# Performance work log

Measured on AMD Instinct MI355X. Metric: run time of the kernel, lower is better.

## Reference

```python
import jax, jax.numpy as jnp
import numpy as np
from math import comb

N_VARS = 6
DEGREE = 4
NUM_TERMS = 768
D1 = DEGREE + 1          # coeffs per variable row (input)
D2 = 2 * DEGREE + 1      # coeffs per variable row after squaring


def _bern_mul_weights(d):
    # Bernstein-basis product: c_k = sum_i C(d,i)C(d,k-i)/C(2d,k) a_i b_{k-i}
    W = np.zeros((d + 1, d + 1, 2 * d + 1), dtype=np.float32)
    for i in range(d + 1):
        for j in range(d + 1):
            W[i, j, i + j] = comb(d, i) * comb(d, j) / comb(2 * d, i + j)
    return W

_W_NP = _bern_mul_weights(DEGREE)          # (D1, D1, D2) product weights
_E_NP = _W_NP.sum(axis=1)                  # (D1, D2) degree elevation d -> 2d (multiply by ones poly)


def ibf_minmax(P):
    """Interval bounds of an implicit-Bernstein-form poly P: (T, V, D1).
    Per term: interval of each var row (Bernstein coeff min/max bound the poly on [0,1]),
    interval product across vars, then interval sum across terms."""
    lo = P.min(-1)  # (T, V)
    hi = P.max(-1)
    T = P.shape[0]
    ones = jnp.ones((T,), P.dtype)

    def step(carry, x):
        clo, chi = carry
        xlo, xhi = x
        cand = jnp.stack([clo * xlo, clo * xhi, chi * xlo, chi * xhi])
        return (cand.min(0), cand.max(0)), None

    (tlo, thi), _ = jax.lax.scan(step, (ones, ones), (lo.T, hi.T))  # scan over V vars
    return tlo.sum(), thi.sum()


def relu_coeffs_under(l, u):
    # quadratic lower relaxation of ReLU on [l,u]: q(x) = (x^2 - l x)/(u - l)
    den = jnp.where(u - l > 0, u - l, jnp.ones_like(u))
    quad = jnp.stack([1.0 / den, -l / den, jnp.zeros_like(l)])
    lin = jnp.array([0.0, 1.0, 0.0], dtype=quad.dtype)
    zero = jnp.zeros(3, dtype=quad.dtype)
    return jnp.where(l >= 0, lin, jnp.where(u <= 0, zero, quad))


def relu_coeffs_over(l, u):
    # quadratic upper relaxation: q(x) = u (x - l)^2 / (u - l)^2
    den = jnp.where(u - l > 0, u - l, jnp.ones_like(u))
    d2 = den * den
    quad = jnp.stack([u / d2, -2.0 * u * l / d2, u * l * l / d2])
    lin = jnp.array([0.0, 1.0, 0.0], dtype=quad.dtype)
    zero = jnp.zeros(3, dtype=quad.dtype)
    return jnp.where(l >= 0, lin, jnp.where(u <= 0, zero, quad))


def quad_of_poly(P, coeffs):
    """Compose quadratic a x^2 + b x + c with IBF poly P (T, V, D1).
    Returns IBF poly with T^2 + T + 1 terms, per-var degree 2*DEGREE."""
    a, b, c = coeffs[0], coeffs[1], coeffs[2]
    W = jnp.asarray(_W_NP)
    E = jnp.asarray(_E_NP)
    T, V, _ = P.shape
    # P^2: all pairwise term products; per-var Bernstein row product
    sq = jnp.einsum('tvi,svj,ijk->tsvk', P, P, W).reshape(T * T, V, D2)
    sq = sq.at[:, 0, :].multiply(a)          # scale by a on first var row
    # b * P: elevate each row from degree d to 2d, scale by b
    lin = jnp.einsum('tvi,ik->tvk', P, E)
    lin = lin.at[:, 0, :].multiply(b)
    # constant term c: all-ones rows, first row scaled by c
    const = jnp.ones((1, V, D2), P.dtype).at[0, 0, :].multiply(c)
    out = jnp.concatenate([sq, lin, const], axis=0)  # (T^2+T+1, V, D2)
    return out.reshape((T * T + T + 1) * V, D2)


def setup_inputs() -> dict:
    key = jax.random.key(0)
    k1, k2 = jax.random.split(key)
    input_under = jax.random.normal(k1, (NUM_TERMS * N_VARS, D1), dtype=jnp.float32)
    input_over = jax.random.normal(k2, (NUM_TERMS * N_VARS, D1), dtype=jnp.float32)
    return {"input_under": input_under, "input_over": input_over}


def reference(input_under, input_over):
    Pu = input_under.reshape(input_under.shape[0] // N_VARS, N_VARS, D1)
    Po = input_over.reshape(input_over.shape[0] // N_VARS, N_VARS, D1)
    l = ibf_minmax(Pu)[0]
    u = ibf_minmax(Po)[1]
    # torch.tensor([l, u]) detaches in the original -> stop_gradient for faithfulness
    l = jax.lax.stop_gradient(l)
    u = jax.lax.stop_gradient(u)
    cu = relu_coeffs_under(l, u)
    co = relu_coeffs_over(l, u)
    relu_node_under = quad_of_poly(Pu, cu)
    relu_node_over = quad_of_poly(Po, co)
    return relu_node_under, relu_node_over
```

## Files before the change

### kernel.cpp

```cpp
#include <hip/hip_runtime.h>

#define T_TERMS 768
#define NV 6
#define D1 5
#define D2 9
#define T2 (T_TERMS * T_TERMS)
#define PTOT (T2 + T_TERMS + 1)
#define NROWS ((unsigned int)PTOT * NV)
#define NOUT (NROWS * (unsigned int)D2)

typedef float f4 __attribute__((ext_vector_type(4)));

__global__ void bounds_kernel(const float* __restrict__ Pu,
                              const float* __restrict__ Po,
                              float* __restrict__ coef) {
    int t = threadIdx.x;
    float tlo = 0.f, thi = 0.f;
    if (t < T_TERMS) {
        float clo_u = 1.f, chi_u = 1.f;
        float clo_o = 1.f, chi_o = 1.f;
        const float* pu = Pu + t * NV * D1;
        const float* po = Po + t * NV * D1;
        #pragma unroll
        for (int v = 0; v < NV; ++v) {
            float lo = pu[v * 5 + 0], hi = lo;
            #pragma unroll
            for (int i = 1; i < 5; ++i) {
                float x = pu[v * 5 + i];
                lo = fminf(lo, x); hi = fmaxf(hi, x);
            }
            float a = clo_u * lo, b = clo_u * hi, c = chi_u * lo, d = chi_u * hi;
            clo_u = fminf(fminf(a, b), fminf(c, d));
            chi_u = fmaxf(fmaxf(a, b), fmaxf(c, d));
            lo = po[v * 5 + 0]; hi = lo;
            #pragma unroll
            for (int i = 1; i < 5; ++i) {
                float x = po[v * 5 + i];
                lo = fminf(lo, x); hi = fmaxf(hi, x);
            }
            a = clo_o * lo; b = clo_o * hi; c = chi_o * lo; d = chi_o * hi;
            clo_o = fminf(fminf(a, b), fminf(c, d));
            chi_o = fmaxf(fmaxf(a, b), fmaxf(c, d));
        }
        tlo = clo_u;
        thi = chi_o;
    }
    __shared__ float slo[12], shi[12];
    for (int off = 32; off; off >>= 1) {
        tlo += __shfl_down(tlo, off);
        thi += __shfl_down(thi, off);
    }
    int wave = threadIdx.x >> 6;
    if ((threadIdx.x & 63) == 0) { slo[wave] = tlo; shi[wave] = thi; }
    __syncthreads();
    if (threadIdx.x == 0) {
        float l = 0.f, u = 0.f;
        #pragma unroll
        for (int w = 0; w < 12; ++w) { l += slo[w]; u += shi[w]; }
        float den = (u - l > 0.f) ? (u - l) : 1.f;
        float au, bu, cu, ao, bo, co;
        if (l >= 0.f) {
            au = 0.f; bu = 1.f; cu = 0.f;
            ao = 0.f; bo = 1.f; co = 0.f;
        } else if (u <= 0.f) {
            au = bu = cu = 0.f;
            ao = bo = co = 0.f;
        } else {
            au = 1.f / den; bu = -l / den; cu = 0.f;
            float d2 = den * den;
            ao = u / d2; bo = -2.f * u * l / d2; co = u * l * l / d2;
        }
        coef[0] = au; coef[1] = bu; coef[2] = cu;
        coef[3] = ao; coef[4] = bo; coef[5] = co;
    }
}

__global__ __launch_bounds__(256) void expand_kernel(
        const float* __restrict__ Pu,
        const float* __restrict__ Po,
        const float* __restrict__ coef,
        float* __restrict__ out) {
    __shared__ float lds[256 * D2];
    static constexpr float Wt[5][5] = {
        {1.0f,        4.0f/8.0f,   6.0f/28.0f,  4.0f/56.0f,  1.0f/70.0f},
        {4.0f/8.0f,   16.0f/28.0f, 24.0f/56.0f, 16.0f/70.0f, 4.0f/56.0f},
        {6.0f/28.0f,  24.0f/56.0f, 36.0f/70.0f, 24.0f/56.0f, 6.0f/28.0f},
        {4.0f/56.0f,  16.0f/70.0f, 24.0f/56.0f, 16.0f/28.0f, 4.0f/8.0f},
        {1.0f/70.0f,  4.0f/56.0f,  6.0f/28.0f,  4.0f/8.0f,   1.0f}
    };

    const unsigned tid = threadIdx.x;
    const unsigned bid = blockIdx.x;
    const unsigned ten = blockIdx.y;
    const float* __restrict__ P = ten ? Po : Pu;
    const float* __restrict__ c3 = coef + ten * 3;

    const unsigned rr = bid * 256u + tid;
    const unsigned nvalid = min(256u, NROWS - bid * 256u);

    float c[9] = {0.f,0.f,0.f,0.f,0.f,0.f,0.f,0.f,0.f};
    if (rr < NROWS) {
        unsigned p = rr / 6u;
        unsigned v = rr - p * 6u;
        float a[5], b[5];
        float scale = 1.f;
        if (p < (unsigned)T2) {
            unsigned t = p / (unsigned)T_TERMS;
            unsigned s = p - t * (unsigned)T_TERMS;
            const float* A = P + (t * NV + v) * D1;
            const float* B = P + (s * NV + v) * D1;
            #pragma unroll
            for (int i = 0; i < 5; ++i) { a[i] = A[i]; b[i] = B[i]; }
            if (v == 0u) scale = c3[0];
        } else if (p < (unsigned)(T2 + T_TERMS)) {
            unsigned t = p - (unsigned)T2;
            const float* A = P + (t * NV + v) * D1;
            #pragma unroll
            for (int i = 0; i < 5; ++i) { a[i] = A[i]; b[i] = 1.f; }
            if (v == 0u) scale = c3[1];
        } else {
            #pragma unroll
            for (int i = 0; i < 5; ++i) { a[i] = 1.f; b[i] = 1.f; }
            if (v == 0u) scale = c3[2];
        }
        #pragma unroll
        for (int i = 0; i < 5; ++i) a[i] *= scale;
        #pragma unroll
        for (int i = 0; i < 5; ++i)
            #pragma unroll
            for (int j = 0; j < 5; ++j)
                c[i + j] = fmaf(Wt[i][j] * a[i], b[j], c[i + j]);
    }
    #pragma unroll
    for (int k = 0; k < 9; ++k) lds[tid * 9u + k] = c[k];
    __syncthreads();

    float* __restrict__ o = out + (size_t)ten * NOUT + (size_t)bid * (256u * D2);
    const unsigned nd = nvalid * 9u;
    if (nvalid == 256u) {
        const f4* l4 = (const f4*)lds;
        f4* o4 = (f4*)o;
        __builtin_nontemporal_store(l4[tid], o4 + tid);
        __builtin_nontemporal_store(l4[tid + 256u], o4 + tid + 256u);
        if (tid < 64u)
            __builtin_nontemporal_store(l4[tid + 512u], o4 + tid + 512u);
    } else {
        for (unsigned x = tid; x < nd; x += 256u)
            __builtin_nontemporal_store(lds[x], o + x);
    }
}

extern "C" void kernel_launch(void* const* d_in, const int* in_sizes, int n_in,
                              void* d_out, int out_size, void* d_ws, size_t ws_size,
                              hipStream_t stream) {
    const float* Pu = (const float*)d_in[0];
    const float* Po = (const float*)d_in[1];
    float* coef = (float*)d_ws;
    float* out = (float*)d_out;

    bounds_kernel<<<1, 768, 0, stream>>>(Pu, Po, coef);

    unsigned int blocks_x = (NROWS + 255u) / 256u;
    dim3 grid(blocks_x, 2, 1);
    expand_kernel<<<grid, 256, 0, stream>>>(Pu, Po, coef, out);
}
```

Before: 268.9 us.

## Restructure expand kernel into 768-thread tiles with LDS-staged operands and aligned stores

The expand kernel now uses 768-thread blocks that each cover one outer term t and 128 inner terms. The inner-term block and the t row are staged cooperatively in LDS, replacing per-thread divisions and scattered global loads. The linear and constant tail rows are handled by separate tail blocks. Output stores drop the nontemporal hint, and the second tensor, whose base is only 8-byte aligned, is written with realigned float4 stores. The bounds kernel also loads each term's rows as float2 vectors. This adds more LDS traffic, an extra barrier, and more complex store indexing.

Measured after the change: 256.5 us. -4.6%, faster.

```diff
diff --git a/kernel.cpp b/kernel.cpp
--- a/kernel.cpp
+++ b/kernel.cpp
@@ -8,42 +8,57 @@
 #define PTOT (T2 + T_TERMS + 1)
 #define NROWS ((unsigned int)PTOT * NV)
 #define NOUT (NROWS * (unsigned int)D2)
+#define SQ_BLOCKS 4608u
+#define TAIL_ROW0 ((unsigned int)T2 * NV)
+#define TAIL_BLOCKS 7u
+#define GRID_X (SQ_BLOCKS + TAIL_BLOCKS)
+#define BLK_DWORDS (768u * D2)
 
 typedef float f4 __attribute__((ext_vector_type(4)));
-
-__global__ void bounds_kernel(const float* __restrict__ Pu,
-                              const float* __restrict__ Po,
-                              float* __restrict__ coef) {
+typedef float f2 __attribute__((ext_vector_type(2)));
+
+__global__ void bounds_coef_kernel(const float* __restrict__ Pu,
+                                   const float* __restrict__ Po,
+                                   float* __restrict__ ws) {
     int t = threadIdx.x;
     float tlo = 0.f, thi = 0.f;
     if (t < T_TERMS) {
-        float clo_u = 1.f, chi_u = 1.f;
-        float clo_o = 1.f, chi_o = 1.f;
-        const float* pu = Pu + t * NV * D1;
-        const float* po = Po + t * NV * D1;
+        f2 r[15];
+        const f2* p2 = (const f2*)(Pu + t * (NV * D1));
+        #pragma unroll
+        for (int i = 0; i < 15; ++i) r[i] = p2[i];
+        const float* rf = (const float*)r;
+        float clo = 1.f, chi = 1.f;
         #pragma unroll
         for (int v = 0; v < NV; ++v) {
-            float lo = pu[v * 5 + 0], hi = lo;
+            float lo = rf[v * 5 + 0], hi = lo;
             #pragma unroll
             for (int i = 1; i < 5; ++i) {
-                float x = pu[v * 5 + i];
+                float x = rf[v * 5 + i];
                 lo = fminf(lo, x); hi = fmaxf(hi, x);
             }
-            float a = clo_u * lo, b = clo_u * hi, c = chi_u * lo, d = chi_u * hi;
-            clo_u = fminf(fminf(a, b), fminf(c, d));
-            chi_u = fmaxf(fmaxf(a, b), fmaxf(c, d));
-            lo = po[v * 5 + 0]; hi = lo;
+            float a = clo * lo, b = clo * hi, c = chi * lo, d = chi * hi;
+            clo = fminf(fminf(a, b), fminf(c, d));
+            chi = fmaxf(fmaxf(a, b), fmaxf(c, d));
+        }
+        tlo = clo;
+        const f2* q2 = (const f2*)(Po + t * (NV * D1));
+        #pragma unroll
+        for (int i = 0; i < 15; ++i) r[i] = q2[i];
+        clo = 1.f; chi = 1.f;
+        #pragma unroll
+        for (int v = 0; v < NV; ++v) {
+            float lo = rf[v * 5 + 0], hi = lo;
             #pragma unroll
             for (int i = 1; i < 5; ++i) {
-                float x = po[v * 5 + i];
+                float x = rf[v * 5 + i];
                 lo = fminf(lo, x); hi = fmaxf(hi, x);
             }
-            a = clo_o * lo; b = clo_o * hi; c = chi_o * lo; d = chi_o * hi;
-            clo_o = fminf(fminf(a, b), fminf(c, d));
-            chi_o = fmaxf(fmaxf(a, b), fmaxf(c, d));
-        }
-        tlo = clo_u;
-        thi = chi_o;
+            float a = clo * lo, b = clo * hi, c = chi * lo, d = chi * hi;
+            clo = fminf(fminf(a, b), fminf(c, d));
+            chi = fmaxf(fmaxf(a, b), fmaxf(c, d));
+        }
+        thi = chi;
     }
     __shared__ float slo[12], shi[12];
     for (int off = 32; off; off >>= 1) {
@@ -70,17 +85,17 @@
             float d2 = den * den;
             ao = u / d2; bo = -2.f * u * l / d2; co = u * l * l / d2;
         }
-        coef[0] = au; coef[1] = bu; coef[2] = cu;
-        coef[3] = ao; coef[4] = bo; coef[5] = co;
+        ws[0] = au; ws[1] = bu; ws[2] = cu;
+        ws[3] = ao; ws[4] = bo; ws[5] = co;
     }
 }
 
-__global__ __launch_bounds__(256) void expand_kernel(
+__global__ __launch_bounds__(768) void expand_kernel(
         const float* __restrict__ Pu,
         const float* __restrict__ Po,
         const float* __restrict__ coef,
         float* __restrict__ out) {
-    __shared__ float lds[256 * D2];
+    __shared__ float lds[BLK_DWORDS + 32];
     static constexpr float Wt[5][5] = {
         {1.0f,        4.0f/8.0f,   6.0f/28.0f,  4.0f/56.0f,  1.0f/70.0f},
         {4.0f/8.0f,   16.0f/28.0f, 24.0f/56.0f, 16.0f/70.0f, 4.0f/56.0f},
@@ -90,39 +105,35 @@
     };
 
     const unsigned tid = threadIdx.x;
-    const unsigned bid = blockIdx.x;
+    const unsigned bx = blockIdx.x;
     const unsigned ten = blockIdx.y;
     const float* __restrict__ P = ten ? Po : Pu;
-    const float* __restrict__ c3 = coef + ten * 3;
-
-    const unsigned rr = bid * 256u + tid;
-    const unsigned nvalid = min(256u, NROWS - bid * 256u);
+    const float sc_sq  = coef[ten * 3 + 0];
+    const float sc_lin = coef[ten * 3 + 1];
+    const float sc_con = coef[ten * 3 + 2];
 
     float c[9] = {0.f,0.f,0.f,0.f,0.f,0.f,0.f,0.f,0.f};
-    if (rr < NROWS) {
-        unsigned p = rr / 6u;
-        unsigned v = rr - p * 6u;
+    bool fullstore = true;
+
+    if (bx < SQ_BLOCKS) {
+        const unsigned t = bx / 6u;
+        const unsigned chunk = bx - t * 6u;
+        const unsigned s0 = chunk * 128u;
+        const float* __restrict__ Bsrc = P + s0 * 30u;
+        #pragma unroll
+        for (unsigned kk = 0; kk < 5; ++kk)
+            lds[tid + 768u * kk] = Bsrc[tid + 768u * kk];
+        if (tid < 30u) lds[BLK_DWORDS + tid] = P[t * 30u + tid];
+        __syncthreads();
+
+        const unsigned s_local = tid / 6u;
+        const unsigned v = tid - s_local * 6u;
         float a[5], b[5];
-        float scale = 1.f;
-        if (p < (unsigned)T2) {
-            unsigned t = p / (unsigned)T_TERMS;
-            unsigned s = p - t * (unsigned)T_TERMS;
-            const float* A = P + (t * NV + v) * D1;
-            const float* B = P + (s * NV + v) * D1;
-            #pragma unroll
-            for (int i = 0; i < 5; ++i) { a[i] = A[i]; b[i] = B[i]; }
-            if (v == 0u) scale = c3[0];
-        } else if (p < (unsigned)(T2 + T_TERMS)) {
-            unsigned t = p - (unsigned)T2;
-            const float* A = P + (t * NV + v) * D1;
-            #pragma unroll
-            for (int i = 0; i < 5; ++i) { a[i] = A[i]; b[i] = 1.f; }
-            if (v == 0u) scale = c3[1];
-        } else {
-            #pragma unroll
-            for (int i = 0; i < 5; ++i) { a[i] = 1.f; b[i] = 1.f; }
-            if (v == 0u) scale = c3[2];
-        }
+        #pragma unroll
+        for (int i = 0; i < 5; ++i) a[i] = lds[BLK_DWORDS + v * 5u + i];
+        #pragma unroll
+        for (int i = 0; i < 5; ++i) b[i] = lds[s_local * 30u + v * 5u + i];
+        const float scale = (v == 0u) ? sc_sq : 1.f;
         #pragma unroll
         for (int i = 0; i < 5; ++i) a[i] *= scale;
         #pragma unroll
@@ -130,23 +141,76 @@
             #pragma unroll
             for (int j = 0; j < 5; ++j)
                 c[i + j] = fmaf(Wt[i][j] * a[i], b[j], c[i + j]);
-    }
+        __syncthreads();
+    } else {
+        const unsigned rbase = TAIL_ROW0 + (bx - SQ_BLOCKS) * 768u;
+        const unsigned r = rbase + tid;
+        if (r < NROWS) {
+            unsigned p = r / 6u;
+            unsigned v = r - p * 6u;
+            float a[5];
+            float scale;
+            if (p < (unsigned)(T2 + T_TERMS)) {
+                unsigned t = p - (unsigned)T2;
+                const float* A = P + (t * 6u + v) * 5u;
+                #pragma unroll
+                for (int i = 0; i < 5; ++i) a[i] = A[i];
+                scale = (v == 0u) ? sc_lin : 1.f;
+            } else {
+                #pragma unroll
+                for (int i = 0; i < 5; ++i) a[i] = 1.f;
+                scale = (v == 0u) ? sc_con : 1.f;
+            }
+            #pragma unroll
+            for (int i = 0; i < 5; ++i) a[i] *= scale;
+            #pragma unroll
+            for (int i = 0; i < 5; ++i)
+                #pragma unroll
+                for (int j = 0; j < 5; ++j)
+                    c[i + j] = fmaf(Wt[i][j], a[i], c[i + j]);
+        }
+        fullstore = (rbase + 768u <= NROWS);
+        __syncthreads();
+    }
+
     #pragma unroll
     for (int k = 0; k < 9; ++k) lds[tid * 9u + k] = c[k];
     __syncthreads();
 
-    float* __restrict__ o = out + (size_t)ten * NOUT + (size_t)bid * (256u * D2);
-    const unsigned nd = nvalid * 9u;
-    if (nvalid == 256u) {
-        const f4* l4 = (const f4*)lds;
-        f4* o4 = (f4*)o;
-        __builtin_nontemporal_store(l4[tid], o4 + tid);
-        __builtin_nontemporal_store(l4[tid + 256u], o4 + tid + 256u);
-        if (tid < 64u)
-            __builtin_nontemporal_store(l4[tid + 512u], o4 + tid + 512u);
+    float* __restrict__ ob = out + (size_t)ten * NOUT + (size_t)bx * BLK_DWORDS;
+    if (fullstore) {
+        if (ten == 0u) {
+            const f4* l4 = (const f4*)lds;
+            f4* o4 = (f4*)ob;
+            o4[tid]          = l4[tid];
+            o4[tid + 768u]   = l4[tid + 768u];
+            if (tid < 192u) o4[tid + 1536u] = l4[tid + 1536u];
+        } else {
+            if (tid < 2u) ob[tid] = lds[tid];
+            if (tid >= 2u && tid < 4u) ob[6908u + tid] = lds[6908u + tid];
+            const f2* l2 = (const f2*)lds;
+            {
+                unsigned q = tid;
+                f2 x = l2[1u + 2u * q], y = l2[2u + 2u * q];
+                f4 vv; vv.x = x.x; vv.y = x.y; vv.z = y.x; vv.w = y.y;
+                *(f4*)(ob + 2u + 4u * q) = vv;
+            }
+            {
+                unsigned q = tid + 768u;
+                f2 x = l2[1u + 2u * q], y = l2[2u + 2u * q];
+                f4 vv; vv.x = x.x; vv.y = x.y; vv.z = y.x; vv.w = y.y;
+                *(f4*)(ob + 2u + 4u * q) = vv;
+            }
+            if (tid < 191u) {
+                unsigned q = tid + 1536u;
+                f2 x = l2[1u + 2u * q], y = l2[2u + 2u * q];
+                f4 vv; vv.x = x.x; vv.y = x.y; vv.z = y.x; vv.w = y.y;
+                *(f4*)(ob + 2u + 4u * q) = vv;
+            }
+        }
     } else {
-        for (unsigned x = tid; x < nd; x += 256u)
-            __builtin_nontemporal_store(lds[x], o + x);
+        const unsigned nd = (NROWS - (TAIL_ROW0 + (bx - SQ_BLOCKS) * 768u)) * 9u;
+        for (unsigned x = tid; x < nd; x += 768u) ob[x] = lds[x];
     }
 }
 
@@ -155,12 +219,11 @@
                               hipStream_t stream) {
     const float* Pu = (const float*)d_in[0];
     const float* Po = (const float*)d_in[1];
-    float* coef = (float*)d_ws;
+    float* ws = (float*)d_ws;
     float* out = (float*)d_out;
 
-    bounds_kernel<<<1, 768, 0, stream>>>(Pu, Po, coef);
-
-    unsigned int blocks_x = (NROWS + 255u) / 256u;
-    dim3 grid(blocks_x, 2, 1);
-    expand_kernel<<<grid, 256, 0, stream>>>(Pu, Po, coef, out);
+    bounds_coef_kernel<<<1, 768, 0, stream>>>(Pu, Po, ws);
+
+    dim3 grid(GRID_X, 2, 1);
+    expand_kernel<<<grid, 768, 0, stream>>>(Pu, Po, ws, out);
 }
```
